# Kernel tuning notes

Hardware: AMD Instinct MI355X
Metric: run time of the kernel (lower is better)

## Reference

```python
import jax, jax.numpy as jnp
import numpy as np

B, T, D, H, O = 512, 256, 128, 256, 128

def _lin(x, W, b):
    # torch Linear: y = x @ W.T + b, W is [out, in]
    return x @ W.T + b

def _n2n(x):
    return jnp.nan_to_num(x, nan=0.0, posinf=0.0, neginf=0.0)

def _forward(x, x_mask, x_delta, noise,
             W_emb, b_emb, W_d1, b_d1, W_d2, b_d2, W_c, b_c,
             W_z, b_z, W_r, b_r, W_h, b_h, ln_g, ln_b, W_o, b_o):
    # input embedding
    x = _n2n(_lin(x, W_emb, b_emb))                       # [B,T,D]
    x_mean = jax.lax.stop_gradient(jnp.mean(x, axis=1))   # [B,D] (detach in torch)
    x_mean = _n2n(x_mean)
    # deltas, clamped (vectorized over T; decay MLP has no recurrence)
    d = jnp.clip(jnp.nan_to_num(x_delta, nan=0.0, posinf=100.0, neginf=0.0), 0.0, 100.0)
    gamma_x = jax.nn.sigmoid(_lin(jax.nn.relu(_lin(d, W_d1, b_d1)), W_d2, b_d2))  # [B,T,D]
    m = x_mask
    x_hat = m * x + (1.0 - m) * (gamma_x * x_mean[:, None, :])
    conf = jax.nn.sigmoid(_lin(jnp.concatenate([x_hat, d], axis=-1), W_c, b_c))   # [B,T,D]
    x_final = _n2n(x_hat * conf + noise * (1.0 - conf))
    # concat [x_final, m, d] is the time-varying part of gate inputs; nan_to_num
    xc = _n2n(jnp.concatenate([x_final, m, d], axis=-1))  # [B,T,3D]
    D3 = 3 * D
    # split gate weights into input-part and hidden-part; precompute input GEMMs
    zx = jnp.einsum('btk,hk->bth', xc, W_z[:, :D3]) + b_z  # [B,T,H]
    rx = jnp.einsum('btk,hk->bth', xc, W_r[:, :D3]) + b_r
    hx = jnp.einsum('btk,hk->bth', xc, W_h[:, :D3]) + b_h
    W_zh, W_rh, W_hh = W_z[:, D3:], W_r[:, D3:], W_h[:, D3:]

    def step(h, inp):
        zx_t, rx_t, hx_t = inp
        z = jax.nn.sigmoid(zx_t + h @ W_zh.T)
        r = jax.nn.sigmoid(rx_t + h @ W_rh.T)
        h_tilde = jnp.tanh(hx_t + (r * h) @ W_hh.T)
        h = _n2n((1.0 - z) * h + z * h_tilde)
        return h, None

    h0 = jnp.zeros((x.shape[0], H), dtype=x.dtype)
    h_last, _ = jax.lax.scan(step, h0, (zx.swapaxes(0, 1), rx.swapaxes(0, 1), hx.swapaxes(0, 1)))
    h_last = _n2n(h_last)
    # output head: LayerNorm(eps=1e-5) -> Dropout(eval: identity) -> Linear
    mu = jnp.mean(h_last, axis=-1, keepdims=True)
    var = jnp.mean((h_last - mu) ** 2, axis=-1, keepdims=True)
    ln = (h_last - mu) / jnp.sqrt(var + 1e-5) * ln_g + ln_b
    return _lin(ln, W_o, b_o)


def setup_inputs() -> dict:
    key = jax.random.key(0)
    ks = jax.random.split(key, 24)
    def W(k, o, i):
        s = 1.0 / np.sqrt(i)
        return jax.random.uniform(k, (o, i), jnp.float32, -s, s)
    def bvec(k, o, i):
        s = 1.0 / np.sqrt(i)
        return jax.random.uniform(k, (o,), jnp.float32, -s, s)
    D3H = 3 * D + H
    return {
        'x': jax.random.normal(ks[0], (B, T, D), jnp.float32),
        'x_mask': (jax.random.uniform(ks[1], (B, T, D)) < 0.8).astype(jnp.float32),
        'x_delta': jax.random.uniform(ks[2], (B, T, D), jnp.float32, 0.0, 10.0),
        'noise': jax.random.normal(ks[3], (B, T, D), jnp.float32),
        'W_emb': W(ks[4], D, D), 'b_emb': bvec(ks[5], D, D),
        'W_d1': W(ks[6], D, D), 'b_d1': bvec(ks[7], D, D),
        'W_d2': W(ks[8], D, D), 'b_d2': bvec(ks[9], D, D),
        'W_c': W(ks[10], D, 2 * D), 'b_c': bvec(ks[11], D, 2 * D),
        'W_z': W(ks[12], H, D3H), 'b_z': bvec(ks[13], H, D3H),
        'W_r': W(ks[14], H, D3H), 'b_r': bvec(ks[15], H, D3H),
        'W_h': W(ks[16], H, D3H), 'b_h': bvec(ks[17], H, D3H),
        'ln_g': jnp.ones((H,), jnp.float32), 'ln_b': jnp.zeros((H,), jnp.float32),
        'W_o': W(ks[18], O, H), 'b_o': bvec(ks[19], O, H),
    }


def reference(x, x_mask, x_delta, noise, W_emb, b_emb, W_d1, b_d1, W_d2, b_d2,
              W_c, b_c, W_z, b_z, W_r, b_r, W_h, b_h, ln_g, ln_b, W_o, b_o):
    return _forward(x, x_mask, x_delta, noise, W_emb, b_emb, W_d1, b_d1, W_d2, b_d2,
                    W_c, b_c, W_z, b_z, W_r, b_r, W_h, b_h, ln_g, ln_b, W_o, b_o)
```

## Files before the change

kernel.cpp:

```cpp
#include <hip/hip_runtime.h>
#include <hip/hip_fp16.h>
#include <math.h>

#define BB 512
#define TT 256
#define DD 128
#define HH 256
#define OO 128
#define KH 640
#define BT (BB*TT)

typedef unsigned int uint_t;
typedef _Float16 f16x8 __attribute__((ext_vector_type(8)));
typedef float f32x4 __attribute__((ext_vector_type(4)));

__device__ __forceinline__ float sigmoidf_(float x){ return 1.0f/(1.0f+__expf(-x)); }
__device__ __forceinline__ float tanhf_(float x){ float e = __expf(-2.0f*x); return 2.0f/(1.0f+e) - 1.0f; }
__device__ __forceinline__ float clipd_(float x){ return fminf(fmaxf(x, 0.f), 100.f); }

typedef _Float16 h2v __attribute__((ext_vector_type(2)));
__device__ __forceinline__ float d2(uint_t a, uint_t b, float c){
#if __has_builtin(__builtin_amdgcn_fdot2)
    return __builtin_amdgcn_fdot2(__builtin_bit_cast(h2v, a), __builtin_bit_cast(h2v, b), c, false);
#else
    __half2 ha = __builtin_bit_cast(__half2, a);
    __half2 hb = __builtin_bit_cast(__half2, b);
    return c + __half2float(ha.x)*__half2float(hb.x) + __half2float(ha.y)*__half2float(hb.y);
#endif
}
__device__ __forceinline__ uint_t pack2(float a, float b){
    __half2 h; h.x = __float2half(a); h.y = __float2half(b);
    return __builtin_bit_cast(uint_t, h);
}

static const size_t SZ_XC   = (size_t)BT*384*2;
static const size_t TAIL_SZ = 589824 + 393216 + 3072 + 262144 + 524288 + 32768*3 + 65536;

__global__ __launch_bounds__(128) void k_wprep(const float* __restrict__ Wz, const float* __restrict__ Wr,
                                               const float* __restrict__ Wh, const float* __restrict__ bz,
                                               const float* __restrict__ br, const float* __restrict__ bh,
                                               __half* __restrict__ Wcat, __half* __restrict__ Wrec,
                                               float* __restrict__ bcat){
    int gj = blockIdx.x; int j = gj & 255;
    const float* src  = (gj < 256 ? Wz : (gj < 512 ? Wr : Wh)) + (size_t)j*KH;
    const float* bsrc = (gj < 256 ? bz : (gj < 512 ? br : bh));
    for(int k=threadIdx.x; k<384; k+=128) Wcat[(size_t)gj*384 + k] = __float2half(src[k]);
    for(int k=threadIdx.x; k<256; k+=128) Wrec[(size_t)gj*256 + k] = __float2half(src[384+k]);
    if(threadIdx.x==0) bcat[gj] = bsrc[j];
}

__global__ __launch_bounds__(256) void k_cvt(const float* __restrict__ a, const float* __restrict__ b,
                                             const float* __restrict__ c, const float* __restrict__ d,
                                             __half* __restrict__ oa, __half* __restrict__ ob,
                                             __half* __restrict__ oc, __half* __restrict__ od){
    int i = blockIdx.x*256 + threadIdx.x;
    if(i < 16384){
        oa[i] = __float2half(a[i]);
        ob[i] = __float2half(b[i]);
        oc[i] = __float2half(c[i]);
    }
    od[i] = __float2half(d[i]);
}

__global__ __launch_bounds__(256,4) void k_embm(const float* __restrict__ x,
                                                const __half* __restrict__ Wh,
                                                const float* __restrict__ bias,
                                                __half* __restrict__ xc){
    __shared__ __align__(16) uint4 TxU[128*16];
    const int tid = threadIdx.x;
    const long row0 = (long)blockIdx.x*128;
    {
        const int srow = tid>>1, shalf = tid&1;
        const long gr = row0 + srow;
        const float4* gx = (const float4*)(x + gr*DD + shalf*64);
        #pragma unroll
        for(int u=0;u<8;++u){
            float4 a = gx[u*2], q = gx[u*2+1];
            uint4 pk;
            pk.x = pack2(a.x,a.y); pk.y = pack2(a.z,a.w);
            pk.z = pack2(q.x,q.y); pk.w = pack2(q.z,q.w);
            int unit = shalf*8 + u;
            TxU[srow*16 + (unit ^ (srow&7))] = pk;
        }
    }
    __syncthreads();
    const int wv = tid>>6, lane = tid&63, g = lane>>4, r16 = lane&15;
    const int wrow0 = wv*32;
    const uint4* WU = (const uint4*)Wh;
    f32x4 acc[2][8];
    #pragma unroll
    for(int i=0;i<2;++i)
        #pragma unroll
        for(int jj=0;jj<8;++jj) acc[i][jj] = (f32x4){0.f,0.f,0.f,0.f};
    #pragma unroll
    for(int ks=0;ks<4;++ks){
        f16x8 af[2], bf[8];
        #pragma unroll
        for(int mf=0;mf<2;++mf){
            int rr = wrow0 + mf*16 + r16;
            af[mf] = __builtin_bit_cast(f16x8, TxU[rr*16 + ((ks*4+g) ^ (rr&7))]);
        }
        #pragma unroll
        for(int nf=0;nf<8;++nf){
            int col = nf*16 + r16;
            bf[nf] = __builtin_bit_cast(f16x8, WU[col*16 + ks*4 + g]);
        }
        #pragma unroll
        for(int mf=0;mf<2;++mf)
            #pragma unroll
            for(int nf=0;nf<8;++nf)
                acc[mf][nf] = __builtin_amdgcn_mfma_f32_16x16x32_f16(af[mf], bf[nf], acc[mf][nf], 0,0,0);
    }
    #pragma unroll
    for(int nf=0;nf<8;++nf){
        int col = nf*16 + r16;
        float bb = bias[col];
        #pragma unroll
        for(int mf=0;mf<2;++mf){
            int rowb = wrow0 + mf*16 + g*4;
            f32x4 v = acc[mf][nf];
            #pragma unroll
            for(int e=0;e<4;++e)
                xc[(size_t)(row0+rowb+e)*384 + col] = __float2half(v[e] + bb);
        }
    }
}

__global__ __launch_bounds__(256) void k_meanv(const __half* __restrict__ xc,
                                               float* __restrict__ xmean){
    __shared__ float red[16][128];
    const int tid = threadIdx.x;
    const int trow = tid>>4, c8 = tid&15;
    const int b = blockIdx.x;
    float s[8];
    #pragma unroll
    for(int e=0;e<8;++e) s[e] = 0.f;
    for(int t=trow; t<TT; t+=16){
        uint4 v = *(const uint4*)(xc + ((size_t)b*TT + t)*384 + c8*8);
        const __half* hp = (const __half*)&v;
        #pragma unroll
        for(int e=0;e<8;++e) s[e] += __half2float(hp[e]);
    }
    #pragma unroll
    for(int e=0;e<8;++e) red[trow][c8*8+e] = s[e];
    __syncthreads();
    if(tid < 128){
        float tot = 0.f;
        #pragma unroll
        for(int r=0;r<16;++r) tot += red[r][tid];
        xmean[b*DD + tid] = tot*(1.0f/TT);
    }
}

__global__ __launch_bounds__(256,2) void k_gatem(__half* __restrict__ xc,
    const float* __restrict__ xmask, const float* __restrict__ xdelta,
    const float* __restrict__ noise,
    const __half* __restrict__ Wd1h, const float* __restrict__ bd1,
    const __half* __restrict__ Wd2h, const float* __restrict__ bd2,
    const __half* __restrict__ Wch,  const float* __restrict__ bc,
    const float* __restrict__ xmean){
    __shared__ __align__(16) uint4 TdU[128*16];
    __shared__ __align__(16) uint4 TtU[128*16];
    __half* Tth = (__half*)TtU;
    const int tid = threadIdx.x;
    const long row0 = (long)blockIdx.x*128;
    const int b = (int)(row0 >> 8);

    {
        const int srow = tid>>1, shalf = tid&1;
        const long gr = row0 + srow;
        const float4* gd = (const float4*)(xdelta + gr*DD + shalf*64);
        const float4* gm = (const float4*)(xmask  + gr*DD + shalf*64);
        uint4* xcu = (uint4*)(xc + gr*384);
        #pragma unroll
        for(int u=0;u<8;++u){
            float4 a = gd[u*2], q = gd[u*2+1];
            uint4 pk;
            pk.x = pack2(clipd_(a.x), clipd_(a.y));
            pk.y = pack2(clipd_(a.z), clipd_(a.w));
            pk.z = pack2(clipd_(q.x), clipd_(q.y));
            pk.w = pack2(clipd_(q.z), clipd_(q.w));
            int unit = shalf*8 + u;
            TdU[srow*16 + (unit ^ (srow&7))] = pk;
            xcu[32 + unit] = pk;
        }
        #pragma unroll
        for(int u=0;u<8;++u){
            float4 a = gm[u*2], q = gm[u*2+1];
            uint4 pk;
            pk.x = pack2(a.x,a.y); pk.y = pack2(a.z,a.w);
            pk.z = pack2(q.x,q.y); pk.w = pack2(q.z,q.w);
            xcu[16 + shalf*8 + u] = pk;
        }
    }
    __syncthreads();

    const int wv = tid>>6, lane = tid&63, g = lane>>4, r16 = lane&15;
    const int wrow0 = wv*32;
    const uint4* W1U = (const uint4*)Wd1h;
    const uint4* W2U = (const uint4*)Wd2h;
    const uint4* WcU = (const uint4*)Wch;
    f32x4 acc[2][8];

    #pragma unroll
    for(int i=0;i<2;++i)
        #pragma unroll
        for(int jj=0;jj<8;++jj) acc[i][jj] = (f32x4){0.f,0.f,0.f,0.f};
    #pragma unroll
    for(int ks=0;ks<4;++ks){
        f16x8 af[2], bf[8];
        #pragma unroll
        for(int mf=0;mf<2;++mf){
            int rr = wrow0 + mf*16 + r16;
            af[mf] = __builtin_bit_cast(f16x8, TdU[rr*16 + ((ks*4+g) ^ (rr&7))]);
        }
        #pragma unroll
        for(int nf=0;nf<8;++nf){
            int col = nf*16 + r16;
            bf[nf] = __builtin_bit_cast(f16x8, W1U[col*16 + ks*4 + g]);
        }
        #pragma unroll
        for(int mf=0;mf<2;++mf)
            #pragma unroll
            for(int nf=0;nf<8;++nf)
                acc[mf][nf] = __builtin_amdgcn_mfma_f32_16x16x32_f16(af[mf], bf[nf], acc[mf][nf], 0,0,0);
    }
    #pragma unroll
    for(int nf=0;nf<8;++nf){
        int col = nf*16 + r16;
        float bb = bd1[col];
        int u = col>>3, cl = col&7;
        #pragma unroll
        for(int mf=0;mf<2;++mf){
            int rowb = wrow0 + mf*16 + g*4;
            f32x4 v = acc[mf][nf];
            #pragma unroll
            for(int e=0;e<4;++e){
                int rr = rowb + e;
                float t = v[e] + bb; t = t > 0.f ? t : 0.f;
                Tth[(rr*16 + (u ^ (rr&7)))*8 + cl] = __float2half(t);
            }
        }
    }

    #pragma unroll
    for(int i=0;i<2;++i)
        #pragma unroll
        for(int jj=0;jj<8;++jj) acc[i][jj] = (f32x4){0.f,0.f,0.f,0.f};
    #pragma unroll
    for(int ks=0;ks<4;++ks){
        f16x8 af[2], bf[8];
        #pragma unroll
        for(int mf=0;mf<2;++mf){
            int rr = wrow0 + mf*16 + r16;
            af[mf] = __builtin_bit_cast(f16x8, TtU[rr*16 + ((ks*4+g) ^ (rr&7))]);
        }
        #pragma unroll
        for(int nf=0;nf<8;++nf){
            int col = nf*16 + r16;
            bf[nf] = __builtin_bit_cast(f16x8, W2U[col*16 + ks*4 + g]);
        }
        #pragma unroll
        for(int mf=0;mf<2;++mf)
            #pragma unroll
            for(int nf=0;nf<8;++nf)
                acc[mf][nf] = __builtin_amdgcn_mfma_f32_16x16x32_f16(af[mf], bf[nf], acc[mf][nf], 0,0,0);
    }

    #pragma unroll
    for(int nf=0;nf<8;++nf){
        int col = nf*16 + r16;
        float b2 = bd2[col];
        float xm = xmean[b*DD + col];
        int u = col>>3, cl = col&7;
        #pragma unroll
        for(int mf=0;mf<2;++mf){
            int rowb = wrow0 + mf*16 + g*4;
            f32x4 v = acc[mf][nf];
            #pragma unroll
            for(int e=0;e<4;++e){
                int rr = rowb + e;
                long grow = row0 + rr;
                float m  = xmask[grow*DD + col];
                float x1 = __half2float(xc[grow*384 + col]);
                float gmm = sigmoidf_(v[e] + b2);
                float xh = m*x1 + (1.f-m)*gmm*xm;
                Tth[(rr*16 + (u ^ (rr&7)))*8 + cl] = __float2half(xh);
            }
        }
    }

    #pragma unroll
    for(int i=0;i<2;++i)
        #pragma unroll
        for(int jj=0;jj<8;++jj) acc[i][jj] = (f32x4){0.f,0.f,0.f,0.f};
    #pragma unroll
    for(int ks=0;ks<4;++ks){
        f16x8 af[2], bf[8];
        #pragma unroll
        for(int mf=0;mf<2;++mf){
            int rr = wrow0 + mf*16 + r16;
            af[mf] = __builtin_bit_cast(f16x8, TtU[rr*16 + ((ks*4+g) ^ (rr&7))]);
        }
        #pragma unroll
        for(int nf=0;nf<8;++nf){
            int col = nf*16 + r16;
            bf[nf] = __builtin_bit_cast(f16x8, WcU[col*32 + ks*4 + g]);
        }
        #pragma unroll
        for(int mf=0;mf<2;++mf)
            #pragma unroll
            for(int nf=0;nf<8;++nf)
                acc[mf][nf] = __builtin_amdgcn_mfma_f32_16x16x32_f16(af[mf], bf[nf], acc[mf][nf], 0,0,0);
    }
    #pragma unroll
    for(int ks=0;ks<4;++ks){
        f16x8 af[2], bf[8];
        #pragma unroll
        for(int mf=0;mf<2;++mf){
            int rr = wrow0 + mf*16 + r16;
            af[mf] = __builtin_bit_cast(f16x8, TdU[rr*16 + ((ks*4+g) ^ (rr&7))]);
        }
        #pragma unroll
        for(int nf=0;nf<8;++nf){
            int col = nf*16 + r16;
            bf[nf] = __builtin_bit_cast(f16x8, WcU[col*32 + 16 + ks*4 + g]);
        }
        #pragma unroll
        for(int mf=0;mf<2;++mf)
            #pragma unroll
            for(int nf=0;nf<8;++nf)
                acc[mf][nf] = __builtin_amdgcn_mfma_f32_16x16x32_f16(af[mf], bf[nf], acc[mf][nf], 0,0,0);
    }

    #pragma unroll
    for(int nf=0;nf<8;++nf){
        int col = nf*16 + r16;
        float bcc = bc[col];
        int u = col>>3, cl = col&7;
        #pragma unroll
        for(int mf=0;mf<2;++mf){
            int rowb = wrow0 + mf*16 + g*4;
            f32x4 v = acc[mf][nf];
            #pragma unroll
            for(int e=0;e<4;++e){
                int rr = rowb + e;
                long grow = row0 + rr;
                float conf = sigmoidf_(v[e] + bcc);
                float xh = __half2float(Tth[(rr*16 + (u ^ (rr&7)))*8 + cl]);
                float nz = noise[grow*DD + col];
                xc[grow*384 + col] = __float2half(xh*conf + nz*(1.f-conf));
            }
        }
    }
}

__global__ __launch_bounds__(256) void k_projm(const __half* __restrict__ xc,
                                               const __half* __restrict__ Wcat,
                                               const float* __restrict__ bcat,
                                               __half* __restrict__ px,
                                               int lTc, int chunk){
    __shared__ __align__(16) __half As[128*64];
    __shared__ __align__(16) __half Bs[128*64];
    const int tid = threadIdx.x;
    const int rblk = blockIdx.x * 128;
    const int ct0  = blockIdx.y * 128;
    const int mTc = (1<<lTc) - 1;

    const int row = tid >> 1;
    const int hf  = tid & 1;
    const int ar  = rblk + row;
    const long grow = ((long)(ar >> lTc))*TT + ((long)chunk << lTc) + (ar & mTc);
    const uint4* gA = (const uint4*)(xc + grow*384);
    const uint4* gB = (const uint4*)(Wcat + (size_t)(ct0 + row)*384);
    uint4* AsU = (uint4*)As;
    uint4* BsU = (uint4*)Bs;

    const int wv = tid >> 6;
    const int wm = wv >> 1, wn = wv & 1;
    const int l  = tid & 63;
    const int g  = l >> 4, r16 = l & 15;

    f32x4 acc[4][4];
    #pragma unroll
    for(int i=0;i<4;++i)
        #pragma unroll
        for(int jj=0;jj<4;++jj) acc[i][jj] = (f32x4){0.f,0.f,0.f,0.f};

    for(int bk=0; bk<6; ++bk){
        uint4 av[4], bv[4];
        #pragma unroll
        for(int u=0;u<4;++u){ av[u] = gA[bk*8 + hf*4 + u]; bv[u] = gB[bk*8 + hf*4 + u]; }
        if(bk) __syncthreads();
        #pragma unroll
        for(int u=0;u<4;++u){
            int uu = hf*4 + u;
            AsU[row*8 + (uu ^ (row&7))] = av[u];
            BsU[row*8 + (uu ^ (row&7))] = bv[u];
        }
        __syncthreads();
        #pragma unroll
        for(int ks=0;ks<2;++ks){
            f16x8 af[4], bf[4];
            #pragma unroll
            for(int mf=0;mf<4;++mf){
                int rr = wm*64 + mf*16 + r16;
                af[mf] = __builtin_bit_cast(f16x8, AsU[rr*8 + ((ks*4+g) ^ (rr&7))]);
            }
            #pragma unroll
            for(int nf=0;nf<4;++nf){
                int rr = wn*64 + nf*16 + r16;
                bf[nf] = __builtin_bit_cast(f16x8, BsU[rr*8 + ((ks*4+g) ^ (rr&7))]);
            }
            #pragma unroll
            for(int mf=0;mf<4;++mf)
                #pragma unroll
                for(int nf=0;nf<4;++nf)
                    acc[mf][nf] = __builtin_amdgcn_mfma_f32_16x16x32_f16(af[mf], bf[nf], acc[mf][nf], 0,0,0);
        }
    }
    #pragma unroll
    for(int nf=0; nf<4; ++nf){
        int col = ct0 + wn*64 + nf*16 + r16;
        float bb = bcat[col];
        #pragma unroll
        for(int mf=0; mf<4; ++mf){
            int r0 = rblk + wm*64 + mf*16 + g*4;
            f32x4 v = acc[mf][nf];
            #pragma unroll
            for(int e=0;e<4;++e)
                px[(size_t)(r0+e)*768 + col] = __float2half(v[e] + bb);
        }
    }
}

__global__ __launch_bounds__(512,2) void k_gruc(const __half* __restrict__ pxc,
                                                const __half* __restrict__ Wrec,
                                                float* __restrict__ hstate,
                                                int Tc, int init){
    __shared__ __align__(16) uint_t hU[2][136];
    __shared__ __align__(16) uint_t rhU[2][136];
    __shared__ __align__(16) uint_t pxs[2][768];
    const int t  = threadIdx.x;
    const int j  = t >> 1;
    const int kh = t & 1;
    const long b0 = (long)blockIdx.x*2;
    const uint_t* Wr32 = (const uint_t*)Wrec;

    uint_t wz[64], wr[64], wh[64];
    #pragma unroll
    for(int q=0;q<64;++q){
        wz[q] = Wr32[(size_t)(      j)*128 + kh*64 + q];
        wr[q] = Wr32[(size_t)(256 + j)*128 + kh*64 + q];
        wh[q] = Wr32[(size_t)(512 + j)*128 + kh*64 + q];
    }

    const uint_t* px32 = (const uint_t*)pxc;
    auto ldpx = [&](int tl, int f)->uint_t{
        int row = (f >= 384); int off = f - row*384;
        return px32[((size_t)(b0+row)*Tc + tl)*384 + off];
    };
    const int hidx = ((j>>7)*136) + (j&127);

    float hreg0, hreg1;
    if(init){ hreg0 = 0.f; hreg1 = 0.f; }
    else    { hreg0 = hstate[(b0+0)*HH + j]; hreg1 = hstate[(b0+1)*HH + j]; }
    if(kh==0){
        ((__half*)hU[0])[hidx] = __float2half(hreg0);
        ((__half*)hU[1])[hidx] = __float2half(hreg1);
    }
    pxs[0][t] = ldpx(0, t);
    if(t < 256) pxs[0][t+512] = ldpx(0, t+512);
    __syncthreads();

    const uint_t* h0p = hU[0]  + kh*68;
    const uint_t* h1p = hU[1]  + kh*68;
    const uint_t* r0p = rhU[0] + kh*68;
    const uint_t* r1p = rhU[1] + kh*68;

    for(int s=0; s<Tc; ++s){
        const int cur = s & 1;
        uint_t nf0 = 0, nf1 = 0;
        if(s < Tc-1){ nf0 = ldpx(s+1, t); if(t < 256) nf1 = ldpx(s+1, t+512); }

        const __half* pxcur = (const __half*)pxs[cur];
        float az0=0.f, az1=0.f, ar0=0.f, ar1=0.f;
        #pragma unroll
        for(int q=0;q<64;q+=4){
            uint4 hv0 = *(const uint4*)(h0p + q);
            uint4 hv1 = *(const uint4*)(h1p + q);
            az0=d2(wz[q+0],hv0.x,az0); ar0=d2(wr[q+0],hv0.x,ar0); az1=d2(wz[q+0],hv1.x,az1); ar1=d2(wr[q+0],hv1.x,ar1);
            az0=d2(wz[q+1],hv0.y,az0); ar0=d2(wr[q+1],hv0.y,ar0); az1=d2(wz[q+1],hv1.y,az1); ar1=d2(wr[q+1],hv1.y,ar1);
            az0=d2(wz[q+2],hv0.z,az0); ar0=d2(wr[q+2],hv0.z,ar0); az1=d2(wz[q+2],hv1.z,az1); ar1=d2(wr[q+2],hv1.z,ar1);
            az0=d2(wz[q+3],hv0.w,az0); ar0=d2(wr[q+3],hv0.w,ar0); az1=d2(wz[q+3],hv1.w,az1); ar1=d2(wr[q+3],hv1.w,ar1);
        }
        az0 += __shfl_xor(az0,1); az1 += __shfl_xor(az1,1);
        ar0 += __shfl_xor(ar0,1); ar1 += __shfl_xor(ar1,1);
        float z0 = sigmoidf_(__half2float(pxcur[        j]) + az0);
        float z1 = sigmoidf_(__half2float(pxcur[768   + j]) + az1);
        float r0 = sigmoidf_(__half2float(pxcur[256   + j]) + ar0);
        float r1 = sigmoidf_(__half2float(pxcur[768+256+j]) + ar1);
        if(kh==0){
            ((__half*)rhU[0])[hidx] = __float2half(r0*hreg0);
            ((__half*)rhU[1])[hidx] = __float2half(r1*hreg1);
        }
        __syncthreads();
        float ah0=0.f, ah1=0.f;
        #pragma unroll
        for(int q=0;q<64;q+=4){
            uint4 rv0 = *(const uint4*)(r0p + q);
            uint4 rv1 = *(const uint4*)(r1p + q);
            ah0=d2(wh[q+0],rv0.x,ah0); ah1=d2(wh[q+0],rv1.x,ah1);
            ah0=d2(wh[q+1],rv0.y,ah0); ah1=d2(wh[q+1],rv1.y,ah1);
            ah0=d2(wh[q+2],rv0.z,ah0); ah1=d2(wh[q+2],rv1.z,ah1);
            ah0=d2(wh[q+3],rv0.w,ah0); ah1=d2(wh[q+3],rv1.w,ah1);
        }
        ah0 += __shfl_xor(ah0,1); ah1 += __shfl_xor(ah1,1);
        float ht0 = tanhf_(__half2float(pxcur[512    + j]) + ah0);
        float ht1 = tanhf_(__half2float(pxcur[768+512+j]) + ah1);
        hreg0 = (1.f - z0)*hreg0 + z0*ht0;
        hreg1 = (1.f - z1)*hreg1 + z1*ht1;
        if(kh==0){
            ((__half*)hU[0])[hidx] = __float2half(hreg0);
            ((__half*)hU[1])[hidx] = __float2half(hreg1);
        }
        if(s < Tc-1){
            pxs[cur^1][t] = nf0;
            if(t < 256) pxs[cur^1][t+512] = nf1;
        }
        __syncthreads();
    }
    if(kh==0){
        hstate[(b0+0)*HH + j] = hreg0;
        hstate[(b0+1)*HH + j] = hreg1;
    }
}

__global__ __launch_bounds__(256) void k_lnout(const float* __restrict__ hbuf,
    const float* __restrict__ lng, const float* __restrict__ lnb,
    const float* __restrict__ Wo, const float* __restrict__ bo,
    float* __restrict__ out){
    __shared__ __align__(16) float ln_s[HH];
    __shared__ float red[8];
    const int b = blockIdx.x, j = threadIdx.x;
    const float v = hbuf[(long)b*HH + j];
    float s = v, ss = v*v;
    const int lane = j & 63, w = j >> 6;
    for(int off=32; off>0; off>>=1){
        s  += __shfl_down(s,  off);
        ss += __shfl_down(ss, off);
    }
    if(lane == 0){ red[w] = s; red[4+w] = ss; }
    __syncthreads();
    float tot  = red[0]+red[1]+red[2]+red[3];
    float tot2 = red[4]+red[5]+red[6]+red[7];
    float mu  = tot  * (1.0f/HH);
    float var = tot2 * (1.0f/HH) - mu*mu;
    float rstd = rsqrtf(var + 1e-5f);
    ln_s[j] = (v - mu)*rstd*lng[j] + lnb[j];
    __syncthreads();
    if(j < OO){
        float acc = bo[j];
        const float4* w4 = (const float4*)(Wo + j*HH);
        const float4* l4 = (const float4*)ln_s;
        for(int k4=0;k4<HH/4;++k4){
            float4 wv = w4[k4], c = l4[k4];
            acc += wv.x*c.x + wv.y*c.y + wv.z*c.z + wv.w*c.w;
        }
        out[(long)b*OO + j] = acc;
    }
}


__global__ __launch_bounds__(128) void k_emb_o(const float* __restrict__ x,
                                               const float* __restrict__ W,
                                               const float* __restrict__ bias,
                                               float* __restrict__ x1){
    __shared__ __align__(16) float xs[8][DD];
    const int j = threadIdx.x;
    const long row0 = (long)blockIdx.x * 32;
    const float bj = bias[j];
    const float4* W4 = (const float4*)(W + j*DD);
    for(int g=0; g<4; ++g){
        const long rbase = row0 + g*8;
        for(int r=0;r<8;++r) xs[r][j] = x[(rbase+r)*DD + j];
        __syncthreads();
        float acc[8];
        #pragma unroll
        for(int r=0;r<8;++r) acc[r] = bj;
        for(int k4=0;k4<DD/4;++k4){
            float4 w = W4[k4];
            #pragma unroll
            for(int r=0;r<8;++r){
                float4 c = ((const float4*)xs[r])[k4];
                acc[r] += c.x*w.x + c.y*w.y + c.z*w.z + c.w*w.w;
            }
        }
        for(int r=0;r<8;++r) x1[(rbase+r)*DD + j] = acc[r];
        __syncthreads();
    }
}

__global__ __launch_bounds__(128) void k_mean_o(const float* __restrict__ x1,
                                                float* __restrict__ xmean){
    const int j = threadIdx.x;
    const int b = blockIdx.x;
    const float* p = x1 + (long)b*TT*DD + j;
    float s = 0.f;
    for(int t=0;t<TT;++t) s += p[(long)t*DD];
    xmean[b*DD + j] = s * (1.0f/TT);
}

__global__ __launch_bounds__(128) void k_gate_o(float* __restrict__ xf,
    const float* __restrict__ xmask, const float* __restrict__ xdelta,
    const float* __restrict__ noise,
    const float* __restrict__ Wd1, const float* __restrict__ bd1,
    const float* __restrict__ Wd2, const float* __restrict__ bd2,
    const float* __restrict__ Wc,  const float* __restrict__ bc,
    const float* __restrict__ xmean){
    __shared__ __align__(16) float ds[8][DD];
    __shared__ __align__(16) float t1s[8][DD];
    __shared__ __align__(16) float xhs[8][DD];
    const int j = threadIdx.x;
    const long row0 = (long)blockIdx.x * 32;
    const int b = (int)(row0 >> 8);
    const float xm = xmean[b*DD + j];
    const float b1 = bd1[j], b2 = bd2[j], bcj = bc[j];
    const float4* Wd1_4 = (const float4*)(Wd1 + j*DD);
    const float4* Wd2_4 = (const float4*)(Wd2 + j*DD);
    const float4* Wc_4  = (const float4*)(Wc  + j*2*DD);
    for(int g=0; g<4; ++g){
        const long rbase = row0 + g*8;
        for(int r=0;r<8;++r)
            ds[r][j] = fminf(fmaxf(xdelta[(rbase+r)*DD + j], 0.f), 100.f);
        __syncthreads();
        float acc[8];
        #pragma unroll
        for(int r=0;r<8;++r) acc[r] = b1;
        for(int k4=0;k4<DD/4;++k4){
            float4 w = Wd1_4[k4];
            #pragma unroll
            for(int r=0;r<8;++r){
                float4 c = ((const float4*)ds[r])[k4];
                acc[r] += c.x*w.x + c.y*w.y + c.z*w.z + c.w*w.w;
            }
        }
        for(int r=0;r<8;++r) t1s[r][j] = fmaxf(acc[r], 0.f);
        __syncthreads();
        #pragma unroll
        for(int r=0;r<8;++r) acc[r] = b2;
        for(int k4=0;k4<DD/4;++k4){
            float4 w = Wd2_4[k4];
            #pragma unroll
            for(int r=0;r<8;++r){
                float4 c = ((const float4*)t1s[r])[k4];
                acc[r] += c.x*w.x + c.y*w.y + c.z*w.z + c.w*w.w;
            }
        }
        for(int r=0;r<8;++r){
            float gmm = sigmoidf_(acc[r]);
            float m  = xmask[(rbase+r)*DD + j];
            float xv = xf[(rbase+r)*DD + j];
            xhs[r][j] = m*xv + (1.f-m)*gmm*xm;
        }
        __syncthreads();
        #pragma unroll
        for(int r=0;r<8;++r) acc[r] = bcj;
        for(int k4=0;k4<DD/4;++k4){
            float4 w = Wc_4[k4];
            #pragma unroll
            for(int r=0;r<8;++r){
                float4 c = ((const float4*)xhs[r])[k4];
                acc[r] += c.x*w.x + c.y*w.y + c.z*w.z + c.w*w.w;
            }
        }
        for(int k4=0;k4<DD/4;++k4){
            float4 w = Wc_4[DD/4 + k4];
            #pragma unroll
            for(int r=0;r<8;++r){
                float4 c = ((const float4*)ds[r])[k4];
                acc[r] += c.x*w.x + c.y*w.y + c.z*w.z + c.w*w.w;
            }
        }
        for(int r=0;r<8;++r){
            float conf = sigmoidf_(acc[r]);
            float xh = xhs[r][j];
            float nz = noise[(rbase+r)*DD + j];
            xf[(rbase+r)*DD + j] = xh*conf + nz*(1.f-conf);
        }
        __syncthreads();
    }
}

__global__ __launch_bounds__(1024) void k_gru_o(const float* __restrict__ xf,
    const float* __restrict__ xmask, const float* __restrict__ xdelta,
    const float* __restrict__ Wz, const float* __restrict__ bz,
    const float* __restrict__ Wr, const float* __restrict__ br,
    const float* __restrict__ Wh, const float* __restrict__ bh,
    float* __restrict__ hout){
    __shared__ __align__(16) float xcs[4][KH];
    __shared__ __align__(16) float rh[4][HH];
    const int tid = threadIdx.x;
    const int j  = tid & 255;
    const int bl = tid >> 8;
    const long bbase = (long)blockIdx.x * 4;
    xcs[bl][384 + j] = 0.f;
    const float bzj = bz[j], brj = br[j], bhj = bh[j];
    const float4* Wz4 = (const float4*)(Wz + (long)j*KH);
    const float4* Wr4 = (const float4*)(Wr + (long)j*KH);
    const float4* Wh4 = (const float4*)(Wh + (long)j*KH);
    __syncthreads();
    for(int t=0;t<TT;++t){
        if(tid < 4*DD){
            int sb = tid >> 7, k = tid & 127;
            long row = (bbase + sb)*TT + t;
            xcs[sb][k]       = xf[row*DD + k];
            xcs[sb][128 + k] = xmask[row*DD + k];
            xcs[sb][256 + k] = fminf(fmaxf(xdelta[row*DD + k], 0.f), 100.f);
        }
        __syncthreads();
        const float4* cb = (const float4*)xcs[bl];
        float az = bzj, ar = brj;
        for(int k4=0;k4<KH/4;++k4){
            float4 wz = Wz4[k4], wrr = Wr4[k4];
            float4 v = cb[k4];
            az += v.x*wz.x + v.y*wz.y + v.z*wz.z + v.w*wz.w;
            ar += v.x*wrr.x + v.y*wrr.y + v.z*wrr.z + v.w*wrr.w;
        }
        float z = sigmoidf_(az);
        float r = sigmoidf_(ar);
        rh[bl][j] = r * xcs[bl][384 + j];
        __syncthreads();
        float ah = bhj;
        for(int k4=0;k4<96;++k4){
            float4 wh = Wh4[k4];
            float4 v = cb[k4];
            ah += v.x*wh.x + v.y*wh.y + v.z*wh.z + v.w*wh.w;
        }
        const float4* rp = (const float4*)rh[bl];
        for(int k4=0;k4<64;++k4){
            float4 wh = Wh4[96 + k4];
            float4 v = rp[k4];
            ah += v.x*wh.x + v.y*wh.y + v.z*wh.z + v.w*wh.w;
        }
        float ht = tanhf(ah);
        float hold = xcs[bl][384 + j];
        float hn = (1.f - z)*hold + z*ht;
        xcs[bl][384 + j] = hn;
        __syncthreads();
    }
    hout[(bbase + bl)*HH + j] = xcs[bl][384 + j];
}


extern "C" void kernel_launch(void* const* d_in, const int* in_sizes, int n_in,
                              void* d_out, int out_size, void* d_ws, size_t ws_size,
                              hipStream_t stream){
    const float* x      = (const float*)d_in[0];
    const float* xmask  = (const float*)d_in[1];
    const float* xdelta = (const float*)d_in[2];
    const float* noise  = (const float*)d_in[3];
    const float* W_emb  = (const float*)d_in[4];
    const float* b_emb  = (const float*)d_in[5];
    const float* W_d1   = (const float*)d_in[6];
    const float* b_d1   = (const float*)d_in[7];
    const float* W_d2   = (const float*)d_in[8];
    const float* b_d2   = (const float*)d_in[9];
    const float* W_c    = (const float*)d_in[10];
    const float* b_c    = (const float*)d_in[11];
    const float* W_z    = (const float*)d_in[12];
    const float* b_z    = (const float*)d_in[13];
    const float* W_r    = (const float*)d_in[14];
    const float* b_r    = (const float*)d_in[15];
    const float* W_h    = (const float*)d_in[16];
    const float* b_h    = (const float*)d_in[17];
    const float* ln_g   = (const float*)d_in[18];
    const float* ln_b   = (const float*)d_in[19];
    const float* W_o    = (const float*)d_in[20];
    const float* b_o    = (const float*)d_in[21];
    float* out = (float*)d_out;
    char* ws = (char*)d_ws;

    int Tc = 0, lTc = 0;
    {
        const int cand[3]  = {128, 64, 32};
        const int lcand[3] = {7, 6, 5};
        for(int i=0;i<3;++i){
            size_t need = SZ_XC + (size_t)cand[i]*786432 + TAIL_SZ;
            if(ws_size >= need){ Tc = cand[i]; lTc = lcand[i]; break; }
        }
    }

    if(Tc > 0){
        __half* xc    = (__half*)(ws);
        char*   p     = ws + SZ_XC;
        __half* pxc   = (__half*)p;              p += (size_t)Tc*786432;
        __half* Wcat  = (__half*)p;              p += 589824;
        __half* Wrec  = (__half*)p;              p += 393216;
        float*  bcat  = (float*)p;               p += 3072;
        float*  xmean = (float*)p;               p += 262144;
        float*  hstate= (float*)p;               p += 524288;
        __half* Wembh = (__half*)p;              p += 32768;
        __half* Wd1h  = (__half*)p;              p += 32768;
        __half* Wd2h  = (__half*)p;              p += 32768;
        __half* Wch   = (__half*)p;

        k_wprep<<<dim3(768),   dim3(128), 0, stream>>>(W_z,W_r,W_h,b_z,b_r,b_h, Wcat, Wrec, bcat);
        k_cvt  <<<dim3(128),   dim3(256), 0, stream>>>(W_emb, W_d1, W_d2, W_c, Wembh, Wd1h, Wd2h, Wch);
        k_embm <<<dim3(BT/128),dim3(256), 0, stream>>>(x, Wembh, b_emb, xc);
        k_meanv<<<dim3(BB),    dim3(256), 0, stream>>>(xc, xmean);
        k_gatem<<<dim3(BT/128),dim3(256), 0, stream>>>(xc, xmask, xdelta, noise,
                                                       Wd1h,b_d1,Wd2h,b_d2,Wch,b_c, xmean);
        const int nchunk = TT / Tc;
        for(int c=0; c<nchunk; ++c){
            k_projm<<<dim3(BB*Tc/128, 6), dim3(256), 0, stream>>>(xc, Wcat, bcat, pxc, lTc, c);
            k_gruc <<<dim3(BB/2), dim3(512), 0, stream>>>(pxc, Wrec, hstate, Tc, c==0 ? 1 : 0);
        }
        k_lnout<<<dim3(BB), dim3(256), 0, stream>>>(hstate, ln_g, ln_b, W_o, b_o, out);
    } else {
        float* xf    = (float*)ws;
        float* xmean = (float*)(ws + (size_t)BT*DD*4);
        float* hbuf  = (float*)(ws + (size_t)BT*DD*4 + (size_t)BB*DD*4);
        k_emb_o  <<<dim3(BT/32), dim3(128), 0, stream>>>(x, W_emb, b_emb, xf);
        k_mean_o <<<dim3(BB),    dim3(128), 0, stream>>>(xf, xmean);
        k_gate_o <<<dim3(BT/32), dim3(128), 0, stream>>>(xf, xmask, xdelta, noise,
                                                         W_d1,b_d1,W_d2,b_d2,W_c,b_c, xmean);
        k_gru_o  <<<dim3(BB/4),  dim3(1024),0, stream>>>(xf, xmask, xdelta,
                                                         W_z,b_z,W_r,b_r,W_h,b_h, hbuf);
        k_lnout  <<<dim3(BB),    dim3(256), 0, stream>>>(hbuf, ln_g, ln_b, W_o, b_o, out);
    }
}
```

Baseline: 1.334 ms.

## Fuse embedding GEMM into gate kernel and compute mean via linearity

The embedding projection is moved into the gate kernel and kept in registers, so the intermediate x1 is no longer written to and read back from the xc buffer. The time mean is now taken over raw x and then pushed through W_emb, which is exact because the projection is linear. This removes one kernel launch and a full pass over the embedded activations. The cost is more register pressure in the fused kernel from the extra 2x8 accumulator array, and the fp32 mean path differs slightly numerically from the fp16 path it replaces.

```diff
diff --git a/kernel.cpp b/kernel.cpp
--- a/kernel.cpp
+++ b/kernel.cpp
@@ -62,17 +62,56 @@
     od[i] = __float2half(d[i]);
 }
 
-__global__ __launch_bounds__(256,4) void k_embm(const float* __restrict__ x,
-                                                const __half* __restrict__ Wh,
-                                                const float* __restrict__ bias,
-                                                __half* __restrict__ xc){
-    __shared__ __align__(16) uint4 TxU[128*16];
+__global__ __launch_bounds__(256) void k_meanx(const float* __restrict__ x,
+                                               const float* __restrict__ Wemb,
+                                               const float* __restrict__ bemb,
+                                               float* __restrict__ xmean){
+    __shared__ float red[2][128];
+    __shared__ __align__(16) float xr[128];
+    const int tid = threadIdx.x;
+    const int b = blockIdx.x;
+    const int col = tid & 127, hf = tid >> 7;
+    float s = 0.f;
+    const float* px = x + ((size_t)b*TT + hf*128)*DD + col;
+    for(int t=0;t<128;++t) s += px[(size_t)t*DD];
+    red[hf][col] = s;
+    __syncthreads();
+    if(tid < 128) xr[tid] = (red[0][tid] + red[1][tid]) * (1.0f/TT);
+    __syncthreads();
+    if(tid < 128){
+        float acc = bemb[tid];
+        const float4* wr = (const float4*)(Wemb + tid*DD);
+        const float4* xv = (const float4*)xr;
+        for(int k4=0;k4<32;++k4){
+            float4 w = wr[k4], v = xv[k4];
+            acc += w.x*v.x + w.y*v.y + w.z*v.z + w.w*v.w;
+        }
+        xmean[b*DD + tid] = acc;
+    }
+}
+
+__global__ __launch_bounds__(256,2) void k_embgate(const float* __restrict__ x,
+    const float* __restrict__ xmask, const float* __restrict__ xdelta,
+    const float* __restrict__ noise,
+    const __half* __restrict__ Wembh, const float* __restrict__ bemb,
+    const __half* __restrict__ Wd1h, const float* __restrict__ bd1,
+    const __half* __restrict__ Wd2h, const float* __restrict__ bd2,
+    const __half* __restrict__ Wch,  const float* __restrict__ bc,
+    const float* __restrict__ xmean, __half* __restrict__ xc){
+    __shared__ __align__(16) uint4 TaU[128*16];
+    __shared__ __align__(16) uint4 TdU[128*16];
+    __half* TaH = (__half*)TaU;
     const int tid = threadIdx.x;
     const long row0 = (long)blockIdx.x*128;
+    const int b = (int)(row0 >> 8);
+
     {
         const int srow = tid>>1, shalf = tid&1;
         const long gr = row0 + srow;
-        const float4* gx = (const float4*)(x + gr*DD + shalf*64);
+        const float4* gx = (const float4*)(x      + gr*DD + shalf*64);
+        const float4* gd = (const float4*)(xdelta + gr*DD + shalf*64);
+        const float4* gm = (const float4*)(xmask  + gr*DD + shalf*64);
+        uint4* xcu = (uint4*)(xc + gr*384);
         #pragma unroll
         for(int u=0;u<8;++u){
             float4 a = gx[u*2], q = gx[u*2+1];
@@ -80,98 +119,8 @@
             pk.x = pack2(a.x,a.y); pk.y = pack2(a.z,a.w);
             pk.z = pack2(q.x,q.y); pk.w = pack2(q.z,q.w);
             int unit = shalf*8 + u;
-            TxU[srow*16 + (unit ^ (srow&7))] = pk;
-        }
-    }
-    __syncthreads();
-    const int wv = tid>>6, lane = tid&63, g = lane>>4, r16 = lane&15;
-    const int wrow0 = wv*32;
-    const uint4* WU = (const uint4*)Wh;
-    f32x4 acc[2][8];
-    #pragma unroll
-    for(int i=0;i<2;++i)
-        #pragma unroll
-        for(int jj=0;jj<8;++jj) acc[i][jj] = (f32x4){0.f,0.f,0.f,0.f};
-    #pragma unroll
-    for(int ks=0;ks<4;++ks){
-        f16x8 af[2], bf[8];
-        #pragma unroll
-        for(int mf=0;mf<2;++mf){
-            int rr = wrow0 + mf*16 + r16;
-            af[mf] = __builtin_bit_cast(f16x8, TxU[rr*16 + ((ks*4+g) ^ (rr&7))]);
-        }
-        #pragma unroll
-        for(int nf=0;nf<8;++nf){
-            int col = nf*16 + r16;
-            bf[nf] = __builtin_bit_cast(f16x8, WU[col*16 + ks*4 + g]);
-        }
-        #pragma unroll
-        for(int mf=0;mf<2;++mf)
-            #pragma unroll
-            for(int nf=0;nf<8;++nf)
-                acc[mf][nf] = __builtin_amdgcn_mfma_f32_16x16x32_f16(af[mf], bf[nf], acc[mf][nf], 0,0,0);
-    }
-    #pragma unroll
-    for(int nf=0;nf<8;++nf){
-        int col = nf*16 + r16;
-        float bb = bias[col];
-        #pragma unroll
-        for(int mf=0;mf<2;++mf){
-            int rowb = wrow0 + mf*16 + g*4;
-            f32x4 v = acc[mf][nf];
-            #pragma unroll
-            for(int e=0;e<4;++e)
-                xc[(size_t)(row0+rowb+e)*384 + col] = __float2half(v[e] + bb);
-        }
-    }
-}
-
-__global__ __launch_bounds__(256) void k_meanv(const __half* __restrict__ xc,
-                                               float* __restrict__ xmean){
-    __shared__ float red[16][128];
-    const int tid = threadIdx.x;
-    const int trow = tid>>4, c8 = tid&15;
-    const int b = blockIdx.x;
-    float s[8];
-    #pragma unroll
-    for(int e=0;e<8;++e) s[e] = 0.f;
-    for(int t=trow; t<TT; t+=16){
-        uint4 v = *(const uint4*)(xc + ((size_t)b*TT + t)*384 + c8*8);
-        const __half* hp = (const __half*)&v;
-        #pragma unroll
-        for(int e=0;e<8;++e) s[e] += __half2float(hp[e]);
-    }
-    #pragma unroll
-    for(int e=0;e<8;++e) red[trow][c8*8+e] = s[e];
-    __syncthreads();
-    if(tid < 128){
-        float tot = 0.f;
-        #pragma unroll
-        for(int r=0;r<16;++r) tot += red[r][tid];
-        xmean[b*DD + tid] = tot*(1.0f/TT);
-    }
-}
-
-__global__ __launch_bounds__(256,2) void k_gatem(__half* __restrict__ xc,
-    const float* __restrict__ xmask, const float* __restrict__ xdelta,
-    const float* __restrict__ noise,
-    const __half* __restrict__ Wd1h, const float* __restrict__ bd1,
-    const __half* __restrict__ Wd2h, const float* __restrict__ bd2,
-    const __half* __restrict__ Wch,  const float* __restrict__ bc,
-    const float* __restrict__ xmean){
-    __shared__ __align__(16) uint4 TdU[128*16];
-    __shared__ __align__(16) uint4 TtU[128*16];
-    __half* Tth = (__half*)TtU;
-    const int tid = threadIdx.x;
-    const long row0 = (long)blockIdx.x*128;
-    const int b = (int)(row0 >> 8);
-
-    {
-        const int srow = tid>>1, shalf = tid&1;
-        const long gr = row0 + srow;
-        const float4* gd = (const float4*)(xdelta + gr*DD + shalf*64);
-        const float4* gm = (const float4*)(xmask  + gr*DD + shalf*64);
-        uint4* xcu = (uint4*)(xc + gr*384);
+            TaU[srow*16 + (unit ^ (srow&7))] = pk;
+        }
         #pragma unroll
         for(int u=0;u<8;++u){
             float4 a = gd[u*2], q = gd[u*2+1];
@@ -197,11 +146,45 @@
 
     const int wv = tid>>6, lane = tid&63, g = lane>>4, r16 = lane&15;
     const int wrow0 = wv*32;
+    const uint4* WeU = (const uint4*)Wembh;
     const uint4* W1U = (const uint4*)Wd1h;
     const uint4* W2U = (const uint4*)Wd2h;
     const uint4* WcU = (const uint4*)Wch;
     f32x4 acc[2][8];
 
+    f32x4 x1f[2][8];
+    #pragma unroll
+    for(int i=0;i<2;++i)
+        #pragma unroll
+        for(int jj=0;jj<8;++jj) x1f[i][jj] = (f32x4){0.f,0.f,0.f,0.f};
+    #pragma unroll
+    for(int ks=0;ks<4;++ks){
+        f16x8 af[2], bf[8];
+        #pragma unroll
+        for(int mf=0;mf<2;++mf){
+            int rr = wrow0 + mf*16 + r16;
+            af[mf] = __builtin_bit_cast(f16x8, TaU[rr*16 + ((ks*4+g) ^ (rr&7))]);
+        }
+        #pragma unroll
+        for(int nf=0;nf<8;++nf){
+            int col = nf*16 + r16;
+            bf[nf] = __builtin_bit_cast(f16x8, WeU[col*16 + ks*4 + g]);
+        }
+        #pragma unroll
+        for(int mf=0;mf<2;++mf)
+            #pragma unroll
+            for(int nf=0;nf<8;++nf)
+                x1f[mf][nf] = __builtin_amdgcn_mfma_f32_16x16x32_f16(af[mf], bf[nf], x1f[mf][nf], 0,0,0);
+    }
+    #pragma unroll
+    for(int nf=0;nf<8;++nf){
+        float bb = bemb[nf*16 + r16];
+        #pragma unroll
+        for(int mf=0;mf<2;++mf)
+            #pragma unroll
+            for(int e=0;e<4;++e) x1f[mf][nf][e] += bb;
+    }
+
     #pragma unroll
     for(int i=0;i<2;++i)
         #pragma unroll
@@ -237,8 +220,8 @@
             #pragma unroll
             for(int e=0;e<4;++e){
                 int rr = rowb + e;
-                float t = v[e] + bb; t = t > 0.f ? t : 0.f;
-                Tth[(rr*16 + (u ^ (rr&7)))*8 + cl] = __float2half(t);
+                float tt = v[e] + bb; tt = tt > 0.f ? tt : 0.f;
+                TaH[(rr*16 + (u ^ (rr&7)))*8 + cl] = __float2half(tt);
             }
         }
     }
@@ -253,7 +236,7 @@
         #pragma unroll
         for(int mf=0;mf<2;++mf){
             int rr = wrow0 + mf*16 + r16;
-            af[mf] = __builtin_bit_cast(f16x8, TtU[rr*16 + ((ks*4+g) ^ (rr&7))]);
+            af[mf] = __builtin_bit_cast(f16x8, TaU[rr*16 + ((ks*4+g) ^ (rr&7))]);
         }
         #pragma unroll
         for(int nf=0;nf<8;++nf){
@@ -282,10 +265,9 @@
                 int rr = rowb + e;
                 long grow = row0 + rr;
                 float m  = xmask[grow*DD + col];
-                float x1 = __half2float(xc[grow*384 + col]);
                 float gmm = sigmoidf_(v[e] + b2);
-                float xh = m*x1 + (1.f-m)*gmm*xm;
-                Tth[(rr*16 + (u ^ (rr&7)))*8 + cl] = __float2half(xh);
+                float xh = m*x1f[mf][nf][e] + (1.f-m)*gmm*xm;
+                TaH[(rr*16 + (u ^ (rr&7)))*8 + cl] = __float2half(xh);
             }
         }
     }
@@ -300,7 +282,7 @@
         #pragma unroll
         for(int mf=0;mf<2;++mf){
             int rr = wrow0 + mf*16 + r16;
-            af[mf] = __builtin_bit_cast(f16x8, TtU[rr*16 + ((ks*4+g) ^ (rr&7))]);
+            af[mf] = __builtin_bit_cast(f16x8, TaU[rr*16 + ((ks*4+g) ^ (rr&7))]);
         }
         #pragma unroll
         for(int nf=0;nf<8;++nf){
@@ -347,7 +329,7 @@
                 int rr = rowb + e;
                 long grow = row0 + rr;
                 float conf = sigmoidf_(v[e] + bcc);
-                float xh = __half2float(Tth[(rr*16 + (u ^ (rr&7)))*8 + cl]);
+                float xh = __half2float(TaH[(rr*16 + (u ^ (rr&7)))*8 + cl]);
                 float nz = noise[grow*DD + col];
                 xc[grow*384 + col] = __float2half(xh*conf + nz*(1.f-conf));
             }
@@ -807,10 +789,10 @@
 
         k_wprep<<<dim3(768),   dim3(128), 0, stream>>>(W_z,W_r,W_h,b_z,b_r,b_h, Wcat, Wrec, bcat);
         k_cvt  <<<dim3(128),   dim3(256), 0, stream>>>(W_emb, W_d1, W_d2, W_c, Wembh, Wd1h, Wd2h, Wch);
-        k_embm <<<dim3(BT/128),dim3(256), 0, stream>>>(x, Wembh, b_emb, xc);
-        k_meanv<<<dim3(BB),    dim3(256), 0, stream>>>(xc, xmean);
-        k_gatem<<<dim3(BT/128),dim3(256), 0, stream>>>(xc, xmask, xdelta, noise,
-                                                       Wd1h,b_d1,Wd2h,b_d2,Wch,b_c, xmean);
+        k_meanx<<<dim3(BB),    dim3(256), 0, stream>>>(x, W_emb, b_emb, xmean);
+        k_embgate<<<dim3(BT/128), dim3(256), 0, stream>>>(x, xmask, xdelta, noise,
+                                                          Wembh, b_emb, Wd1h, b_d1,
+                                                          Wd2h, b_d2, Wch, b_c, xmean, xc);
         const int nchunk = TT / Tc;
         for(int c=0; c<nchunk; ++c){
             k_projm<<<dim3(BB*Tc/128, 6), dim3(256), 0, stream>>>(xc, Wcat, bcat, pxc, lTc, c);
```

Result: no change. 1.360 ms (+1.9%).
